# Optimization experiments

Measured on AMD Instinct MI355X. Metric: run time of the kernel, lower is better.

The kernel has to match this reference:

```python
import jax, jax.numpy as jnp
import numpy as np

B, DIM, L, H, W = 4, 128, 256, 8, 8
N = L * H * W
D_INNER, D_STATE, D_CONV, DT_RANK = 128, 8, 4, 8


def _ln(x, w, b, eps=1e-5):
    m = x.mean(-1, keepdims=True)
    v = ((x - m) ** 2).mean(-1, keepdims=True)
    return (x - m) * jax.lax.rsqrt(v + eps) * w + b


def _mamba_fusion(x, z_in, p, i):
    # x, z_in: (B, N, DIM). x drives the SSM; z_in provides the cross-modal gate.
    u = x @ p['Wx'][i]                                    # (B, N, D_INNER)
    z = z_in @ p['Wz'][i]                                 # (B, N, D_INNER)
    # causal depthwise conv1d along tokens, kernel D_CONV (torch pad=k-1 then truncate)
    up = jnp.pad(u, ((0, 0), (D_CONV - 1, 0), (0, 0)))
    w = p['conv_w'][i]                                    # (D_INNER, D_CONV)
    uc = sum(up[:, k:k + u.shape[1], :] * w[:, k] for k in range(D_CONV)) + p['conv_b'][i]
    uc = jax.nn.silu(uc)
    x_dbl = uc @ p['Wxproj'][i]                           # (B, N, DT_RANK + 2*D_STATE)
    dt_r, Bm, Cm = jnp.split(x_dbl, [DT_RANK, DT_RANK + D_STATE], axis=-1)
    dt = jax.nn.softplus(dt_r @ p['Wdt'][i] + p['bdt'][i])  # (B, N, D_INNER)
    A = -jnp.exp(p['A_log'][i])                           # (D_INNER, D_STATE)
    dA = jnp.exp(dt[..., None] * A)                       # (B, N, D_INNER, D_STATE)
    dBu = dt[..., None] * Bm[:, :, None, :] * uc[..., None]

    def step(h, inp):
        dA_t, dBu_t, C_t = inp
        h = dA_t * h + dBu_t                              # (B, D_INNER, D_STATE)
        return h, jnp.einsum('bds,bs->bd', h, C_t)

    h0 = jnp.zeros((u.shape[0], D_INNER, D_STATE), u.dtype)
    _, ys = jax.lax.scan(step, h0, (dA.swapaxes(0, 1), dBu.swapaxes(0, 1), Cm.swapaxes(0, 1)))
    y = ys.swapaxes(0, 1) + p['Dp'][i] * uc
    y = y * jax.nn.silu(z)
    return y @ p['Wout_m'][i] + p['bout_m'][i]


def _cross_block(in0, in1, p, i):
    skip = in0
    a = _ln(in0, p['ln0_w'][i], p['ln0_b'][i])
    b = _ln(in1, p['ln1_w'][i], p['ln1_b'][i])
    return skip + _mamba_fusion(a, b, p, i)


def setup_inputs() -> dict:
    key = jax.random.key(0)
    ks = jax.random.split(key, 16)
    s_in = 1.0 / np.sqrt(DIM)
    s_di = 1.0 / np.sqrt(D_INNER)
    inp = {
        'front': jax.random.normal(ks[0], (B, DIM, L, H, W), jnp.float32),
        'back': jax.random.normal(ks[1], (B, DIM, L, H, W), jnp.float32),
        'ln0_w': jnp.ones((2, DIM), jnp.float32),
        'ln0_b': jnp.zeros((2, DIM), jnp.float32),
        'ln1_w': jnp.ones((2, DIM), jnp.float32),
        'ln1_b': jnp.zeros((2, DIM), jnp.float32),
        'Wx': jax.random.normal(ks[2], (2, DIM, D_INNER), jnp.float32) * s_in,
        'Wz': jax.random.normal(ks[3], (2, DIM, D_INNER), jnp.float32) * s_in,
        'conv_w': jax.random.normal(ks[4], (2, D_INNER, D_CONV), jnp.float32) * 0.5,
        'conv_b': jnp.zeros((2, D_INNER), jnp.float32),
        'Wxproj': jax.random.normal(ks[5], (2, D_INNER, DT_RANK + 2 * D_STATE), jnp.float32) * s_di,
        'Wdt': jax.random.normal(ks[6], (2, DT_RANK, D_INNER), jnp.float32) * (1.0 / np.sqrt(DT_RANK)),
        'bdt': jnp.full((2, D_INNER), -4.6, jnp.float32),  # softplus^-1(~0.01)
        'A_log': jnp.broadcast_to(jnp.log(jnp.arange(1, D_STATE + 1, dtype=jnp.float32)), (2, D_INNER, D_STATE)).copy(),
        'Dp': jnp.ones((2, D_INNER), jnp.float32),
        'Wout_m': jax.random.normal(ks[7], (2, D_INNER, DIM), jnp.float32) * s_di,
        'bout_m': jnp.zeros((2, DIM), jnp.float32),
        'Wout': jax.random.normal(ks[8], (DIM, DIM), jnp.float32) * s_in,
        'bout': jnp.zeros((DIM,), jnp.float32),
    }
    return inp


def reference(front, back, ln0_w, ln0_b, ln1_w, ln1_b, Wx, Wz, conv_w, conv_b,
              Wxproj, Wdt, bdt, A_log, Dp, Wout_m, bout_m, Wout, bout):
    p = dict(ln0_w=ln0_w, ln0_b=ln0_b, ln1_w=ln1_w, ln1_b=ln1_b, Wx=Wx, Wz=Wz,
             conv_w=conv_w, conv_b=conv_b, Wxproj=Wxproj, Wdt=Wdt, bdt=bdt,
             A_log=A_log, Dp=Dp, Wout_m=Wout_m, bout_m=bout_m)
    ff = front.reshape(B, DIM, N).swapaxes(1, 2)          # (B, N, DIM)
    bf = back.reshape(B, DIM, N).swapaxes(1, 2)
    f_fus = _cross_block(ff, bf, p, 0)
    b_fus = _cross_block(bf, ff, p, 1)
    fusion = ((f_fus + b_fus) * 0.5) @ Wout + bout
    return fusion.swapaxes(1, 2).reshape(B, DIM, L, H, W)
```

## Files before the change

kernel.cpp:

```cpp
#include <hip/hip_runtime.h>

#define DEV static __device__ __forceinline__

typedef short s16x8 __attribute__((ext_vector_type(8)));
typedef float f32x4 __attribute__((ext_vector_type(4)));
typedef unsigned short u16;

DEV float b2f(u16 u){ return __uint_as_float(((unsigned int)u) << 16); }
DEV u16 f2b(float f){
  unsigned int x = __float_as_uint(f);
  x += 0x7fffu + ((x >> 16) & 1u);
  return (u16)(x >> 16);
}
DEV float silu_f(float x){ return x * __builtin_amdgcn_rcpf(1.f + __expf(-x)); }
DEV float softplus_f(float x){ return (x > 15.f) ? x : __logf(1.f + __expf(x)); }
DEV bool detf32(const void* lnw){ return *(const unsigned int*)lnw == 0x3F800000u; }
DEV float ldin(const void* p, long long i, bool f){
  return f ? ((const float*)p)[i] : b2f(((const u16*)p)[i]);
}

static constexpr int BATCH = 4;
static constexpr int NSEQ  = 16384;
static constexpr int RTOT  = BATCH * NSEQ;
static constexpr int GCH   = 256;
static constexpr int DIRSZ = BATCH*GCH*128*8;

__global__ __launch_bounds__(256) void k_setup(
                        const void* ln0w, const void* ln0b, const void* ln1w, const void* ln1b,
                        const void* Wx, const void* Wz, const void* Wxp, const void* Wdt,
                        const void* bdt, const void* Alog, const void* convw, const void* convb,
                        const void* Dpr, const void* Woutm, const void* boutm,
                        const void* Wout, const void* bout,
                        u16* Wuz, u16* WdtBC, u16* Wcat, u16* WoutT,
                        float* buz, float* bdtf, float* bcat, float* boutf,
                        float* Aexp, float* convwF, float* convbF, float* DpF)
{
  bool f = detf32(ln0w);
  int tid = blockIdx.x * 256 + threadIdx.x;
  int gs  = gridDim.x * 256;
  for (int idx = tid; idx < 2*256*128; idx += gs){
    int d = idx >> 15; int n = (idx >> 7) & 255; int k = idx & 127;
    float wv;
    if (n < 128) wv = ldin(ln0w, d*128+k, f) * ldin(Wx, (long long)(d*128+k)*128 + n, f);
    else         wv = ldin(ln1w, (1-d)*128+k, f) * ldin(Wz, (long long)((1-d)*128+k)*128 + (n-128), f);
    Wuz[idx] = f2b(wv);
  }
  for (int idx = tid; idx < 2*256; idx += gs){
    int d = idx >> 8; int n = idx & 255;
    float s = 0.f;
    if (n < 128){
      for (int k = 0; k < 128; ++k)
        s += ldin(ln0b, d*128+k, f) * ldin(Wx, (long long)(d*128+k)*128 + n, f);
    } else {
      for (int k = 0; k < 128; ++k)
        s += ldin(ln1b, (1-d)*128+k, f) * ldin(Wz, (long long)((1-d)*128+k)*128 + (n-128), f);
    }
    buz[idx] = s;
  }
  for (int idx = tid; idx < 2*128; idx += gs)
    bdtf[idx] = ldin(bdt, idx, f);
  for (int idx = tid; idx < 2*144*128; idx += gs){
    int i = idx / (144*128); int rem = idx % (144*128); int n = rem >> 7; int k = rem & 127;
    if (n < 128){
      float s = 0.f;
      for (int j = 0; j < 8; ++j)
        s += ldin(Wxp, (long long)(i*128+k)*24 + j, f) * ldin(Wdt, (long long)(i*8+j)*128 + n, f);
      WdtBC[idx] = f2b(s);
    } else {
      WdtBC[idx] = f2b(ldin(Wxp, (long long)(i*128+k)*24 + (n - 120), f));
    }
  }
  for (int idx = tid; idx < 128*256; idx += gs){
    int n = idx >> 8; int k = idx & 255;
    Wcat[idx] = f2b(ldin(Woutm, (long long)k*128 + n, f));
  }
  for (int idx = tid; idx < 128*128; idx += gs){
    int n = idx >> 7, k = idx & 127;
    WoutT[idx] = f2b(ldin(Wout, (long long)k*128 + n, f));
  }
  for (int idx = tid; idx < 128; idx += gs){
    bcat[idx]  = ldin(boutm, idx, f) + ldin(boutm, 128 + idx, f);
    boutf[idx] = ldin(bout, idx, f);
  }
  for (int idx = tid; idx < 2*128*8; idx += gs)
    Aexp[idx] = -expf(ldin(Alog, idx, f));
  for (int idx = tid; idx < 2*128*4; idx += gs)
    convwF[idx] = ldin(convw, idx, f);
  for (int idx = tid; idx < 2*128; idx += gs){
    convbF[idx] = ldin(convb, idx, f);
    DpF[idx]   = ldin(Dpr, idx, f);
  }
}

__global__ __launch_bounds__(256) void k_ln(const void* front, const void* back, const void* ln0w,
                                            u16* xf, u16* xb, u16* sfbh)
{
  bool fF = detf32(ln0w);
  __shared__ u16 Af[64][130];
  __shared__ u16 Ab[64][130];
  __shared__ float Mf[64], Rf[64], Mb[64], Rb[64];
  int tid = threadIdx.x;
  long long r0 = (long long)blockIdx.x * 64;
  int b  = (int)(r0 >> 14);
  int n0 = (int)(r0 & 16383);
  if (fF){
    const float* fp = (const float*)front;
    const float* bp = (const float*)back;
    for (int it = 0; it < 8; ++it){
      int d = it*16 + (tid >> 4);
      int t = (tid & 15) * 4;
      long long gi = ((long long)(b*128 + d))*NSEQ + n0 + t;
      float4 vf = *(const float4*)&fp[gi];
      float4 vb = *(const float4*)&bp[gi];
      Af[t+0][d] = f2b(vf.x); Af[t+1][d] = f2b(vf.y);
      Af[t+2][d] = f2b(vf.z); Af[t+3][d] = f2b(vf.w);
      Ab[t+0][d] = f2b(vb.x); Ab[t+1][d] = f2b(vb.y);
      Ab[t+2][d] = f2b(vb.z); Ab[t+3][d] = f2b(vb.w);
    }
  } else {
    const u16* fp = (const u16*)front;
    const u16* bp = (const u16*)back;
    for (int it = 0; it < 4; ++it){
      int d = it*32 + (tid >> 3);
      int t = (tid & 7) * 8;
      long long gi = ((long long)(b*128 + d))*NSEQ + n0 + t;
      uint4 vf = *(const uint4*)&fp[gi];
      uint4 vb = *(const uint4*)&bp[gi];
      Af[t+0][d] = (u16)vf.x; Af[t+1][d] = (u16)(vf.x>>16);
      Af[t+2][d] = (u16)vf.y; Af[t+3][d] = (u16)(vf.y>>16);
      Af[t+4][d] = (u16)vf.z; Af[t+5][d] = (u16)(vf.z>>16);
      Af[t+6][d] = (u16)vf.w; Af[t+7][d] = (u16)(vf.w>>16);
      Ab[t+0][d] = (u16)vb.x; Ab[t+1][d] = (u16)(vb.x>>16);
      Ab[t+2][d] = (u16)vb.y; Ab[t+3][d] = (u16)(vb.y>>16);
      Ab[t+4][d] = (u16)vb.z; Ab[t+5][d] = (u16)(vb.z>>16);
      Ab[t+6][d] = (u16)vb.w; Ab[t+7][d] = (u16)(vb.w>>16);
    }
  }
  __syncthreads();
  {
    int t = tid >> 2, sub = tid & 3;
    float s = 0.f, ss = 0.f, s2 = 0.f, ss2 = 0.f;
    for (int k = 0; k < 32; ++k){
      float v = b2f(Af[t][sub*32 + k]); s  += v; ss  += v*v;
      float w = b2f(Ab[t][sub*32 + k]); s2 += w; ss2 += w*w;
    }
    for (int m = 1; m < 4; m <<= 1){
      s  += __shfl_xor(s,  m, 64); ss  += __shfl_xor(ss,  m, 64);
      s2 += __shfl_xor(s2, m, 64); ss2 += __shfl_xor(ss2, m, 64);
    }
    if (sub == 0){
      float mf = s  * (1.f/128.f); float vf = ss  * (1.f/128.f) - mf*mf;
      Mf[t] = mf; Rf[t] = rsqrtf(vf + 1e-5f);
      float mb = s2 * (1.f/128.f); float vb = ss2 * (1.f/128.f) - mb*mb;
      Mb[t] = mb; Rb[t] = rsqrtf(vb + 1e-5f);
    }
  }
  __syncthreads();
  for (int it = 0; it < 8; ++it){
    int t = it*8 + (tid >> 5);
    int c = (tid & 31) * 4;
    float mf = Mf[t], rf = Rf[t], mb = Mb[t], rb = Rb[t];
    float f0 = b2f(Af[t][c+0]), f1 = b2f(Af[t][c+1]), f2 = b2f(Af[t][c+2]), f3 = b2f(Af[t][c+3]);
    float g0 = b2f(Ab[t][c+0]), g1 = b2f(Ab[t][c+1]), g2 = b2f(Ab[t][c+2]), g3 = b2f(Ab[t][c+3]);
    ushort4 xo, zo, so;
    xo.x = f2b((f0-mf)*rf); xo.y = f2b((f1-mf)*rf); xo.z = f2b((f2-mf)*rf); xo.w = f2b((f3-mf)*rf);
    zo.x = f2b((g0-mb)*rb); zo.y = f2b((g1-mb)*rb); zo.z = f2b((g2-mb)*rb); zo.w = f2b((g3-mb)*rb);
    so.x = f2b(f0+g0); so.y = f2b(f1+g1); so.z = f2b(f2+g2); so.w = f2b(f3+g3);
    long long o = (r0 + t)*128 + c;
    *(ushort4*)&xf[o] = xo;
    *(ushort4*)&xb[o] = zo;
    *(ushort4*)&sfbh[o] = so;
  }
}

__global__ __launch_bounds__(256) void k_guz(const u16* __restrict__ xf,
                                             const u16* __restrict__ xb,
                                             const u16* __restrict__ Wuz,
                                             const float* __restrict__ buz,
                                             u16* __restrict__ u0, u16* __restrict__ u1,
                                             u16* __restrict__ z0, u16* __restrict__ z1)
{
  int dir = blockIdx.y;
  const u16* A = dir ? xb : xf;
  const u16* Wt = Wuz + dir*256*128;
  const float* bias = buz + dir*256;
  u16* outU = dir ? u1 : u0;
  u16* outZ = dir ? z0 : z1;
  __shared__ u16 Wl[256][72];
  __shared__ u16 Al[64][72];
  int tid = threadIdx.x;
  long long r0 = (long long)blockIdx.x * 64;
  int w = tid >> 6, lane = tid & 63;
  int q = lane >> 4, m = lane & 15;
  f32x4 acc[16];
  #pragma unroll
  for (int ct = 0; ct < 16; ++ct) acc[ct] = (f32x4){0.f,0.f,0.f,0.f};
  for (int kp = 0; kp < 2; ++kp){
    if (kp) __syncthreads();
    for (int ci = tid; ci < 256*8; ci += 256){
      int n = ci >> 3, c8 = ci & 7;
      *(uint4*)&Wl[n][c8*8] = *(const uint4*)&Wt[n*128 + kp*64 + c8*8];
    }
    for (int ci = tid; ci < 64*8; ci += 256){
      int rl = ci >> 3, c8 = ci & 7;
      *(uint4*)&Al[rl][c8*8] = *(const uint4*)&A[(r0 + rl)*128 + kp*64 + c8*8];
    }
    __syncthreads();
    #pragma unroll
    for (int kt = 0; kt < 2; ++kt){
      s16x8 af = *(const s16x8*)&Al[w*16 + m][kt*32 + q*8];
      #pragma unroll
      for (int ct = 0; ct < 16; ++ct){
        s16x8 bf = *(const s16x8*)&Wl[ct*16 + m][kt*32 + q*8];
        acc[ct] = __builtin_amdgcn_mfma_f32_16x16x32_bf16(af, bf, acc[ct], 0, 0, 0);
      }
    }
  }
  #pragma unroll
  for (int ct = 0; ct < 16; ++ct){
    int col = ct*16 + m;
    #pragma unroll
    for (int i = 0; i < 4; ++i){
      long long r = r0 + w*16 + q*4 + i;
      float v = acc[ct][i] + bias[col];
      if (col < 128) outU[r*128 + col] = f2b(v);
      else           outZ[r*128 + (col - 128)] = f2b(silu_f(v));
    }
  }
}

__global__ __launch_bounds__(256) void k_cps(const u16* __restrict__ u0p,
                                             const u16* __restrict__ u1p,
                                             const float* __restrict__ convwF,
                                             const float* __restrict__ convbF,
                                             const u16* __restrict__ WdtBC,
                                             const float* __restrict__ bdtf,
                                             const float* __restrict__ Aexp,
                                             u16* __restrict__ uc0p, u16* __restrict__ uc1p,
                                             u16* __restrict__ yg,
                                             float* __restrict__ BCg,
                                             float* __restrict__ P, float* __restrict__ Q)
{
  __shared__ u16 Al[64][136];
  __shared__ u16 Wl[144][136];
  __shared__ float BCl[64][16];
  int dir = blockIdx.y;
  const u16* u = dir ? u1p : u0p;
  u16* ucb = dir ? uc1p : uc0p;
  const u16* Wt = WdtBC + dir*18432;
  const float* bias = bdtf + dir*128;
  u16* dtb = yg + dir*128;
  float* BC = BCg + (long long)dir*RTOT*16;
  int tid = threadIdx.x;
  long long r0 = (long long)blockIdx.x * 64;
  int b  = (int)(r0 >> 14);
  int n0 = (int)(r0 & 16383);
  for (int ci = tid; ci < 144*16; ci += 256){
    int n = ci >> 4, c8 = ci & 15;
    *(uint4*)&Wl[n][c8*8] = *(const uint4*)&Wt[n*128 + c8*8];
  }
  {
    int c = tid & 127, h = tid >> 7;
    const float* wp = &convwF[(dir*128 + c)*4];
    float w0 = wp[0], w1 = wp[1], w2 = wp[2], w3 = wp[3];
    float cb = convbF[dir*128 + c];
    int t0 = h*32;
    const u16* up = u + (long long)b*NSEQ*128 + c;
    int nbase = n0 + t0;
    float win0 = (nbase-3 >= 0) ? b2f(up[(long long)(nbase-3)*128]) : 0.f;
    float win1 = (nbase-2 >= 0) ? b2f(up[(long long)(nbase-2)*128]) : 0.f;
    float win2 = (nbase-1 >= 0) ? b2f(up[(long long)(nbase-1)*128]) : 0.f;
    #pragma unroll
    for (int t = 0; t < 32; ++t){
      float cur = b2f(up[(long long)(nbase + t)*128]);
      float a = win0*w0 + win1*w1 + win2*w2 + cur*w3 + cb;
      u16 s = f2b(silu_f(a));
      Al[t0 + t][c] = s;
      ucb[(r0 + t0 + t)*128 + c] = s;
      win0 = win1; win1 = win2; win2 = cur;
    }
  }
  __syncthreads();
  int w = tid >> 6, lane = tid & 63;
  int q = lane >> 4, m = lane & 15;
  f32x4 acc[9];
  #pragma unroll
  for (int ct = 0; ct < 9; ++ct) acc[ct] = (f32x4){0.f,0.f,0.f,0.f};
  #pragma unroll
  for (int kt = 0; kt < 4; ++kt){
    s16x8 af = *(const s16x8*)&Al[w*16 + m][kt*32 + q*8];
    #pragma unroll
    for (int ct = 0; ct < 9; ++ct){
      s16x8 bf = *(const s16x8*)&Wl[ct*16 + m][kt*32 + q*8];
      acc[ct] = __builtin_amdgcn_mfma_f32_16x16x32_bf16(af, bf, acc[ct], 0, 0, 0);
    }
  }
  __syncthreads();
  u16* Dl = (u16*)&Wl[0][0];
  #pragma unroll
  for (int ct = 0; ct < 9; ++ct){
    int col = ct*16 + m;
    #pragma unroll
    for (int i = 0; i < 4; ++i){
      int rl = w*16 + q*4 + i;
      long long r = r0 + rl;
      float v = acc[ct][i];
      if (col < 128){
        u16 dv = f2b(softplus_f(v + bias[col]));
        dtb[r*256 + col] = dv;
        Dl[rl*136 + col] = dv;
      } else {
        BC[r*16 + (col - 128)] = v;
        BCl[rl][col - 128] = v;
      }
    }
  }
  __syncthreads();
  {
    int c = tid & 127, sh = tid >> 7;
    int g = (int)(r0 & 16383) >> 6;
    float Ac[4], Pr[4], H[4];
    #pragma unroll
    for (int j = 0; j < 4; ++j){
      Ac[j] = Aexp[(dir*128 + c)*8 + sh*4 + j];
      Pr[j] = 1.f; H[j] = 0.f;
    }
    for (int t = 0; t < 64; ++t){
      float d  = b2f(Dl[t*136 + c]);
      float uu = b2f(Al[t][c]);
      float du = d * uu;
      #pragma unroll
      for (int j = 0; j < 4; ++j){
        float dA = __expf(d * Ac[j]);
        H[j]  = dA*H[j] + du*BCl[t][sh*4 + j];
        Pr[j] *= dA;
      }
    }
    long long o = (long long)dir*DIRSZ + (((long long)b*GCH + g)*128 + c)*8 + sh*4;
    *(float4*)&P[o] = make_float4(Pr[0],Pr[1],Pr[2],Pr[3]);
    *(float4*)&Q[o] = make_float4(H[0],H[1],H[2],H[3]);
  }
}

__global__ __launch_bounds__(64) void k_scan2(const float* __restrict__ P,
                                              const float* __restrict__ Q,
                                              float* __restrict__ hinit)
{
  int idx = blockIdx.x*64 + threadIdx.x;
  int dir = idx >> 12;
  int rem = idx & 4095;
  int b  = rem >> 10;
  int cs = rem & 1023;
  long long base = (long long)dir*DIRSZ + (long long)b*GCH*1024 + cs;
  float h = 0.f;
  for (int g = 0; g < GCH; g += 8){
    long long o = base + (long long)g*1024;
    float p[8], qv[8];
    #pragma unroll
    for (int j = 0; j < 8; ++j){ p[j] = P[o + j*1024]; qv[j] = Q[o + j*1024]; }
    #pragma unroll
    for (int j = 0; j < 8; ++j){
      hinit[o + j*1024] = h;
      h = p[j]*h + qv[j];
    }
  }
}

__global__ __launch_bounds__(256) void k_scan3(const u16* __restrict__ uc0p,
                                               const u16* __restrict__ uc1p,
                                               const float* __restrict__ BCg,
                                               const float* __restrict__ hinit,
                                               const u16* __restrict__ z0p,
                                               const u16* __restrict__ z1p,
                                               const float* __restrict__ DpF,
                                               const float* __restrict__ Aexp,
                                               u16* yg)
{
  __shared__ float Bl[128][8];
  __shared__ float Cl[128][8];
  int dir = blockIdx.y;
  const u16* uc = dir ? uc1p : uc0p;
  const u16* zs = dir ? z1p : z0p;
  const float* BC = BCg + (long long)dir*RTOT*16;
  int tid = threadIdx.x;
  int gp = blockIdx.x & 127;
  int b  = blockIdx.x >> 7;
  long long tokbase = (long long)b*NSEQ + gp*128;
  for (int idx = tid; idx < 128*8; idx += 256){
    int row = idx >> 3, s = idx & 7;
    Bl[row][s] = BC[(tokbase + row)*16 + s];
    Cl[row][s] = BC[(tokbase + row)*16 + 8 + s];
  }
  __syncthreads();
  int c = tid & 127;
  int gh = tid >> 7;
  int g = gp*2 + gh;
  int doff = dir*128;
  float Ac[8], H[8];
  long long ho = (long long)dir*DIRSZ + (((long long)b*GCH + g)*128 + c)*8;
  float4 h0 = *(const float4*)&hinit[ho];
  float4 h1 = *(const float4*)&hinit[ho + 4];
  H[0]=h0.x; H[1]=h0.y; H[2]=h0.z; H[3]=h0.w;
  H[4]=h1.x; H[5]=h1.y; H[6]=h1.z; H[7]=h1.w;
  #pragma unroll
  for (int s = 0; s < 8; ++s) Ac[s] = Aexp[(dir*128 + c)*8 + s];
  float dpc = DpF[dir*128 + c];
  long long rbase = (long long)b*NSEQ + g*64;
  for (int t = 0; t < 64; ++t){
    long long r = rbase + t;
    float d  = b2f(yg[r*256 + doff + c]);
    float uu = b2f(uc[r*128 + c]);
    float du = d * uu;
    int rowl = gh*64 + t;
    float y = 0.f;
    #pragma unroll
    for (int s = 0; s < 8; ++s){
      float dA = __expf(d * Ac[s]);
      H[s] = dA*H[s] + du*Bl[rowl][s];
      y += H[s]*Cl[rowl][s];
    }
    float zv = b2f(zs[r*128 + c]);
    yg[r*256 + doff + c] = f2b((y + dpc*uu) * zv);
  }
}

__global__ __launch_bounds__(256) void k_tail(const u16* __restrict__ yg,
                                              const u16* __restrict__ Wcat,
                                              const float* __restrict__ bcat,
                                              const u16* __restrict__ sfbh,
                                              const u16* __restrict__ WoutT,
                                              const float* __restrict__ boutf,
                                              void* outp, const void* dflag)
{
  __shared__ u16 Wl[128][136];
  __shared__ u16 Al[64][136];
  __shared__ u16 Sl[64][136];
  int tid = threadIdx.x;
  long long r0 = (long long)blockIdx.x * 64;
  int w = tid >> 6, lane = tid & 63;
  int q = lane >> 4, m = lane & 15;
  f32x4 acc[8];
  #pragma unroll
  for (int ct = 0; ct < 8; ++ct) acc[ct] = (f32x4){0.f,0.f,0.f,0.f};
  for (int kp = 0; kp < 2; ++kp){
    if (kp) __syncthreads();
    for (int ci = tid; ci < 128*16; ci += 256){
      int n = ci >> 4, c8 = ci & 15;
      *(uint4*)&Wl[n][c8*8] = *(const uint4*)&Wcat[n*256 + kp*128 + c8*8];
    }
    for (int ci = tid; ci < 64*16; ci += 256){
      int rl = ci >> 4, c8 = ci & 15;
      *(uint4*)&Al[rl][c8*8] = *(const uint4*)&yg[(r0 + rl)*256 + kp*128 + c8*8];
    }
    __syncthreads();
    #pragma unroll
    for (int kt = 0; kt < 4; ++kt){
      s16x8 af = *(const s16x8*)&Al[w*16 + m][kt*32 + q*8];
      #pragma unroll
      for (int ct = 0; ct < 8; ++ct){
        s16x8 bf = *(const s16x8*)&Wl[ct*16 + m][kt*32 + q*8];
        acc[ct] = __builtin_amdgcn_mfma_f32_16x16x32_bf16(af, bf, acc[ct], 0, 0, 0);
      }
    }
  }
  #pragma unroll
  for (int ct = 0; ct < 8; ++ct){
    int col = ct*16 + m;
    #pragma unroll
    for (int i = 0; i < 4; ++i){
      int rl = w*16 + q*4 + i;
      long long r = r0 + rl;
      Sl[rl][col] = f2b(acc[ct][i] + bcat[col] + b2f(sfbh[r*128 + col]));
    }
  }
  __syncthreads();
  for (int ci = tid; ci < 128*16; ci += 256){
    int n = ci >> 4, c8 = ci & 15;
    *(uint4*)&Wl[n][c8*8] = *(const uint4*)&WoutT[n*128 + c8*8];
  }
  __syncthreads();
  f32x4 acc2[8];
  #pragma unroll
  for (int ct = 0; ct < 8; ++ct) acc2[ct] = (f32x4){0.f,0.f,0.f,0.f};
  #pragma unroll
  for (int kt = 0; kt < 4; ++kt){
    s16x8 af = *(const s16x8*)&Sl[w*16 + m][kt*32 + q*8];
    #pragma unroll
    for (int ct = 0; ct < 8; ++ct){
      s16x8 bf = *(const s16x8*)&Wl[ct*16 + m][kt*32 + q*8];
      acc2[ct] = __builtin_amdgcn_mfma_f32_16x16x32_bf16(af, bf, acc2[ct], 0, 0, 0);
    }
  }
  u16* Tl = &Al[0][0];
  #pragma unroll
  for (int ct = 0; ct < 8; ++ct){
    int col = ct*16 + m;
    #pragma unroll
    for (int i = 0; i < 4; ++i){
      int rl = w*16 + q*4 + i;
      Tl[col*68 + rl] = f2b(0.5f*acc2[ct][i] + boutf[col]);
    }
  }
  __syncthreads();
  long long b = r0 >> 14; long long tok0 = r0 & 16383;
  bool fo = detf32(dflag);
  if (fo){
    float* of = (float*)outp;
    for (int idx = tid; idx < 128*16; idx += 256){
      int n = idx >> 4; int t0 = (idx & 15)*4;
      float4 v;
      v.x = b2f(Tl[n*68 + t0+0]); v.y = b2f(Tl[n*68 + t0+1]);
      v.z = b2f(Tl[n*68 + t0+2]); v.w = b2f(Tl[n*68 + t0+3]);
      *(float4*)&of[(((long long)(b*128 + n)) << 14) + tok0 + t0] = v;
    }
  } else {
    u16* ob = (u16*)outp;
    for (int idx = tid; idx < 128*16; idx += 256){
      int n = idx >> 4; int t0 = (idx & 15)*4;
      ushort4 v;
      v.x = Tl[n*68 + t0+0]; v.y = Tl[n*68 + t0+1];
      v.z = Tl[n*68 + t0+2]; v.w = Tl[n*68 + t0+3];
      *(ushort4*)&ob[(((long long)(b*128 + n)) << 14) + tok0 + t0] = v;
    }
  }
}

extern "C" void kernel_launch(void* const* d_in, const int* in_sizes, int n_in,
                              void* d_out, int out_size, void* d_ws, size_t ws_size,
                              hipStream_t stream)
{
  (void)in_sizes; (void)n_in; (void)out_size; (void)ws_size;
  const void* front = d_in[0];
  const void* back  = d_in[1];
  const void* ln0w  = d_in[2];
  const void* ln0b  = d_in[3];
  const void* ln1w  = d_in[4];
  const void* ln1b  = d_in[5];
  const void* Wx    = d_in[6];
  const void* Wz    = d_in[7];
  const void* convw = d_in[8];
  const void* convb = d_in[9];
  const void* Wxp   = d_in[10];
  const void* Wdt   = d_in[11];
  const void* bdt   = d_in[12];
  const void* Alog  = d_in[13];
  const void* Dpr   = d_in[14];
  const void* Woutm = d_in[15];
  const void* boutm = d_in[16];
  const void* Wout  = d_in[17];
  const void* bout  = d_in[18];

  char* p = (char*)d_ws;
  auto alloc = [&](size_t bytes) -> void* {
    void* q = (void*)p; p += (bytes + 255) & ~(size_t)255; return q;
  };
  u16*   xf    = (u16*)  alloc((size_t)RTOT*128*2);
  u16*   xb    = (u16*)  alloc((size_t)RTOT*128*2);
  u16*   sfbh  = (u16*)  alloc((size_t)RTOT*128*2);
  u16*   u0    = (u16*)  alloc((size_t)RTOT*128*2);
  u16*   u1    = (u16*)  alloc((size_t)RTOT*128*2);
  u16*   z0    = (u16*)  alloc((size_t)RTOT*128*2);
  u16*   z1    = (u16*)  alloc((size_t)RTOT*128*2);
  float* BC    = (float*)alloc((size_t)2*RTOT*16*4);
  float* Pb    = (float*)alloc((size_t)2*DIRSZ*4);
  float* Qb    = (float*)alloc((size_t)2*DIRSZ*4);
  float* hin   = (float*)alloc((size_t)2*DIRSZ*4);
  u16*   yg    = (u16*)  alloc((size_t)RTOT*256*2);
  u16*   Wuz   = (u16*)  alloc(2*256*128*2);
  u16*   WdtBC = (u16*)  alloc(2*144*128*2);
  u16*   Wcat  = (u16*)  alloc(128*256*2);
  u16*   WoutT = (u16*)  alloc(128*128*2);
  float* buz   = (float*)alloc(2*256*4);
  float* bdtf  = (float*)alloc(2*128*4);
  float* bcat  = (float*)alloc(128*4);
  float* boutf = (float*)alloc(128*4);
  float* Aexp  = (float*)alloc(2*128*8*4);
  float* convwF= (float*)alloc(2*128*4*4);
  float* convbF= (float*)alloc(2*128*4);
  float* DpF   = (float*)alloc(2*128*4);

  k_setup<<<128,256,0,stream>>>(ln0w,ln0b,ln1w,ln1b,Wx,Wz,Wxp,Wdt,bdt,Alog,convw,convb,Dpr,
                                Woutm,boutm,Wout,bout,
                                Wuz,WdtBC,Wcat,WoutT,buz,bdtf,bcat,boutf,Aexp,
                                convwF,convbF,DpF);
  k_ln<<<RTOT/64,256,0,stream>>>(front,back,ln0w,xf,xb,sfbh);

  dim3 g2(RTOT/64, 2);
  k_guz<<<g2,256,0,stream>>>(xf, xb, Wuz, buz, u0, u1, z0, z1);
  k_cps<<<g2,256,0,stream>>>(u0, u1, convwF, convbF, WdtBC, bdtf, Aexp,
                             xf, xb, yg, BC, Pb, Qb);
  k_scan2<<<128,64,0,stream>>>(Pb, Qb, hin);
  dim3 g3(BATCH*GCH/2, 2);
  k_scan3<<<g3,256,0,stream>>>(xf, xb, BC, hin, z0, z1, DpF, Aexp, yg);
  k_tail<<<RTOT/64,256,0,stream>>>(yg, Wcat, bcat, sfbh, WoutT, boutf, d_out, ln0w);
}
```

Before: 347.5 us.

## Widen chunk-scan parallelism, use exp2 with prescaled A, transpose LDS tiles

k_cps now runs 512 threads per block. It splits the conv across four 16-token segments and the MFMA columns across two warp groups. The chunk-local scan uses a swizzled transposed LDS layout and two states per thread, and computes the decay product as exp2(A*sum(dt)) instead of a running product. k_scan3 launches one block per 64-token chunk with two lanes per channel, each holding four states, and combines them with a shuffle. A is premultiplied by log2(e) so exp2 replaces exp. The intent is to raise occupancy and parallelism in the scan stages, at the cost of more blocks, shuffles and LDS aliasing complexity.

```diff
diff --git a/kernel.cpp b/kernel.cpp
--- a/kernel.cpp
+++ b/kernel.cpp
@@ -23,7 +23,7 @@
 static constexpr int NSEQ  = 16384;
 static constexpr int RTOT  = BATCH * NSEQ;
 static constexpr int GCH   = 256;
-static constexpr int DIRSZ = BATCH*GCH*128*8;
+static constexpr long long DIRSZ = (long long)BATCH*GCH*128*8;
 
 __global__ __launch_bounds__(256) void k_setup(
                         const void* ln0w, const void* ln0b, const void* ln1w, const void* ln1b,
@@ -33,7 +33,7 @@
                         const void* Wout, const void* bout,
                         u16* Wuz, u16* WdtBC, u16* Wcat, u16* WoutT,
                         float* buz, float* bdtf, float* bcat, float* boutf,
-                        float* Aexp, float* convwF, float* convbF, float* DpF)
+                        float* Aexp2, float* convwF, float* convbF, float* DpF)
 {
   bool f = detf32(ln0w);
   int tid = blockIdx.x * 256 + threadIdx.x;
@@ -83,7 +83,7 @@
     boutf[idx] = ldin(bout, idx, f);
   }
   for (int idx = tid; idx < 2*128*8; idx += gs)
-    Aexp[idx] = -expf(ldin(Alog, idx, f));
+    Aexp2[idx] = -expf(ldin(Alog, idx, f)) * 1.44269504f;
   for (int idx = tid; idx < 2*128*4; idx += gs)
     convwF[idx] = ldin(convw, idx, f);
   for (int idx = tid; idx < 2*128; idx += gs){
@@ -229,13 +229,26 @@
   }
 }
 
-__global__ __launch_bounds__(256) void k_cps(const u16* __restrict__ u0p,
+DEV uint4 pack8(const u16* v){
+  uint4 r;
+  r.x = (unsigned)v[0] | ((unsigned)v[1]<<16);
+  r.y = (unsigned)v[2] | ((unsigned)v[3]<<16);
+  r.z = (unsigned)v[4] | ((unsigned)v[5]<<16);
+  r.w = (unsigned)v[6] | ((unsigned)v[7]<<16);
+  return r;
+}
+DEV void unpack8(uint4 v, u16* o){
+  o[0]=(u16)v.x; o[1]=(u16)(v.x>>16); o[2]=(u16)v.y; o[3]=(u16)(v.y>>16);
+  o[4]=(u16)v.z; o[5]=(u16)(v.z>>16); o[6]=(u16)v.w; o[7]=(u16)(v.w>>16);
+}
+
+__global__ __launch_bounds__(512) void k_cps(const u16* __restrict__ u0p,
                                              const u16* __restrict__ u1p,
                                              const float* __restrict__ convwF,
                                              const float* __restrict__ convbF,
                                              const u16* __restrict__ WdtBC,
                                              const float* __restrict__ bdtf,
-                                             const float* __restrict__ Aexp,
+                                             const float* __restrict__ Aexp2,
                                              u16* __restrict__ uc0p, u16* __restrict__ uc1p,
                                              u16* __restrict__ yg,
                                              float* __restrict__ BCg,
@@ -243,7 +256,9 @@
 {
   __shared__ u16 Al[64][136];
   __shared__ u16 Wl[144][136];
-  __shared__ float BCl[64][16];
+  __shared__ uint4 UcT4[128*8];
+  float* BCs = (float*)&Al[0][0];
+  uint4* DlT4 = (uint4*)&Wl[0][0];
   int dir = blockIdx.y;
   const u16* u = dir ? u1p : u0p;
   u16* ucb = dir ? uc1p : uc0p;
@@ -255,7 +270,7 @@
   long long r0 = (long long)blockIdx.x * 64;
   int b  = (int)(r0 >> 14);
   int n0 = (int)(r0 & 16383);
-  for (int ci = tid; ci < 144*16; ci += 256){
+  for (int ci = tid; ci < 144*16; ci += 512){
     int n = ci >> 4, c8 = ci & 15;
     *(uint4*)&Wl[n][c8*8] = *(const uint4*)&Wt[n*128 + c8*8];
   }
@@ -264,81 +279,110 @@
     const float* wp = &convwF[(dir*128 + c)*4];
     float w0 = wp[0], w1 = wp[1], w2 = wp[2], w3 = wp[3];
     float cb = convbF[dir*128 + c];
-    int t0 = h*32;
+    int t0 = h*16;
     const u16* up = u + (long long)b*NSEQ*128 + c;
     int nbase = n0 + t0;
     float win0 = (nbase-3 >= 0) ? b2f(up[(long long)(nbase-3)*128]) : 0.f;
     float win1 = (nbase-2 >= 0) ? b2f(up[(long long)(nbase-2)*128]) : 0.f;
     float win2 = (nbase-1 >= 0) ? b2f(up[(long long)(nbase-1)*128]) : 0.f;
-    #pragma unroll
-    for (int t = 0; t < 32; ++t){
+    u16 tmp[16];
+    #pragma unroll
+    for (int t = 0; t < 16; ++t){
       float cur = b2f(up[(long long)(nbase + t)*128]);
       float a = win0*w0 + win1*w1 + win2*w2 + cur*w3 + cb;
       u16 s = f2b(silu_f(a));
+      tmp[t] = s;
       Al[t0 + t][c] = s;
       ucb[(r0 + t0 + t)*128 + c] = s;
       win0 = win1; win1 = win2; win2 = cur;
     }
+    UcT4[c*8 + ((h*2+0) ^ (c&7))] = pack8(tmp);
+    UcT4[c*8 + ((h*2+1) ^ (c&7))] = pack8(tmp+8);
   }
   __syncthreads();
   int w = tid >> 6, lane = tid & 63;
   int q = lane >> 4, m = lane & 15;
-  f32x4 acc[9];
-  #pragma unroll
-  for (int ct = 0; ct < 9; ++ct) acc[ct] = (f32x4){0.f,0.f,0.f,0.f};
+  int rt = w & 3;
+  int cg = w >> 2;
+  int ct0 = cg ? 5 : 0;
+  int nct = cg ? 4 : 5;
+  f32x4 acc[5];
+  #pragma unroll
+  for (int j = 0; j < 5; ++j) acc[j] = (f32x4){0.f,0.f,0.f,0.f};
   #pragma unroll
   for (int kt = 0; kt < 4; ++kt){
-    s16x8 af = *(const s16x8*)&Al[w*16 + m][kt*32 + q*8];
-    #pragma unroll
-    for (int ct = 0; ct < 9; ++ct){
-      s16x8 bf = *(const s16x8*)&Wl[ct*16 + m][kt*32 + q*8];
-      acc[ct] = __builtin_amdgcn_mfma_f32_16x16x32_bf16(af, bf, acc[ct], 0, 0, 0);
-    }
-  }
-  __syncthreads();
-  u16* Dl = (u16*)&Wl[0][0];
-  #pragma unroll
-  for (int ct = 0; ct < 9; ++ct){
-    int col = ct*16 + m;
-    #pragma unroll
-    for (int i = 0; i < 4; ++i){
-      int rl = w*16 + q*4 + i;
-      long long r = r0 + rl;
-      float v = acc[ct][i];
-      if (col < 128){
-        u16 dv = f2b(softplus_f(v + bias[col]));
-        dtb[r*256 + col] = dv;
-        Dl[rl*136 + col] = dv;
-      } else {
-        BC[r*16 + (col - 128)] = v;
-        BCl[rl][col - 128] = v;
+    s16x8 af = *(const s16x8*)&Al[rt*16 + m][kt*32 + q*8];
+    #pragma unroll
+    for (int j = 0; j < 5; ++j){
+      if (j < nct){
+        s16x8 bf = *(const s16x8*)&Wl[(ct0+j)*16 + m][kt*32 + q*8];
+        acc[j] = __builtin_amdgcn_mfma_f32_16x16x32_bf16(af, bf, acc[j], 0, 0, 0);
       }
     }
   }
   __syncthreads();
+  int rl0 = rt*16 + q*4;
+  #pragma unroll
+  for (int j = 0; j < 5; ++j){
+    if (j >= nct) continue;
+    int col = (ct0+j)*16 + m;
+    if (col < 128){
+      ushort4 dv;
+      u16 dd[4];
+      #pragma unroll
+      for (int i = 0; i < 4; ++i){
+        u16 v = f2b(softplus_f(acc[j][i] + bias[col]));
+        dd[i] = v;
+        dtb[(r0 + rl0 + i)*256 + col] = v;
+      }
+      dv.x=dd[0]; dv.y=dd[1]; dv.z=dd[2]; dv.w=dd[3];
+      u16* d16 = (u16*)DlT4;
+      *(ushort4*)&d16[((col*8 + ((rl0>>3) ^ (col&7)))<<3) + (rl0&7)] = dv;
+    } else {
+      int s = col - 128;
+      #pragma unroll
+      for (int i = 0; i < 4; ++i)
+        BC[(r0 + rl0 + i)*16 + s] = acc[j][i];
+      float4 bv; bv.x=acc[j][0]; bv.y=acc[j][1]; bv.z=acc[j][2]; bv.w=acc[j][3];
+      *(float4*)&BCs[s*68 + rl0] = bv;
+    }
+  }
+  __syncthreads();
   {
-    int c = tid & 127, sh = tid >> 7;
+    int c = tid & 127, sq = tid >> 7;
+    int s0 = sq*2;
+    float Ac0 = Aexp2[(dir*128 + c)*8 + s0];
+    float Ac1 = Aexp2[(dir*128 + c)*8 + s0 + 1];
+    float H0 = 0.f, H1 = 0.f, sd = 0.f;
+    #pragma unroll
+    for (int g8 = 0; g8 < 8; ++g8){
+      int gi = c*8 + (g8 ^ (c&7));
+      u16 uu8[8], dd8[8];
+      unpack8(UcT4[gi], uu8);
+      unpack8(DlT4[gi], dd8);
+      float4 b0a = *(const float4*)&BCs[s0*68 + g8*8];
+      float4 b0b = *(const float4*)&BCs[s0*68 + g8*8 + 4];
+      float4 b1a = *(const float4*)&BCs[(s0+1)*68 + g8*8];
+      float4 b1b = *(const float4*)&BCs[(s0+1)*68 + g8*8 + 4];
+      const float* p0 = &b0a.x;
+      const float* p1 = &b1a.x;
+      #pragma unroll
+      for (int jj = 0; jj < 8; ++jj){
+        float d  = b2f(dd8[jj]);
+        float du = d * b2f(uu8[jj]);
+        sd += d;
+        float B0 = (jj < 4) ? p0[jj] : (&b0b.x)[jj-4];
+        float B1 = (jj < 4) ? p1[jj] : (&b1b.x)[jj-4];
+        H0 = __builtin_exp2f(d*Ac0)*H0 + du*B0;
+        H1 = __builtin_exp2f(d*Ac1)*H1 + du*B1;
+      }
+    }
     int g = (int)(r0 & 16383) >> 6;
-    float Ac[4], Pr[4], H[4];
-    #pragma unroll
-    for (int j = 0; j < 4; ++j){
-      Ac[j] = Aexp[(dir*128 + c)*8 + sh*4 + j];
-      Pr[j] = 1.f; H[j] = 0.f;
-    }
-    for (int t = 0; t < 64; ++t){
-      float d  = b2f(Dl[t*136 + c]);
-      float uu = b2f(Al[t][c]);
-      float du = d * uu;
-      #pragma unroll
-      for (int j = 0; j < 4; ++j){
-        float dA = __expf(d * Ac[j]);
-        H[j]  = dA*H[j] + du*BCl[t][sh*4 + j];
-        Pr[j] *= dA;
-      }
-    }
-    long long o = (long long)dir*DIRSZ + (((long long)b*GCH + g)*128 + c)*8 + sh*4;
-    *(float4*)&P[o] = make_float4(Pr[0],Pr[1],Pr[2],Pr[3]);
-    *(float4*)&Q[o] = make_float4(H[0],H[1],H[2],H[3]);
+    long long o = (long long)dir*DIRSZ + (((long long)b*GCH + g)*128 + c)*8 + s0;
+    P[o]   = __builtin_exp2f(Ac0*sd);
+    P[o+1] = __builtin_exp2f(Ac1*sd);
+    Q[o]   = H0;
+    Q[o+1] = H1;
   }
 }
 
@@ -373,54 +417,56 @@
                                                const u16* __restrict__ z0p,
                                                const u16* __restrict__ z1p,
                                                const float* __restrict__ DpF,
-                                               const float* __restrict__ Aexp,
+                                               const float* __restrict__ Aexp2,
                                                u16* yg)
 {
-  __shared__ float Bl[128][8];
-  __shared__ float Cl[128][8];
+  __shared__ float Bl[64][8];
+  __shared__ float Cl[64][8];
   int dir = blockIdx.y;
   const u16* uc = dir ? uc1p : uc0p;
   const u16* zs = dir ? z1p : z0p;
   const float* BC = BCg + (long long)dir*RTOT*16;
   int tid = threadIdx.x;
-  int gp = blockIdx.x & 127;
-  int b  = blockIdx.x >> 7;
-  long long tokbase = (long long)b*NSEQ + gp*128;
-  for (int idx = tid; idx < 128*8; idx += 256){
+  int b = blockIdx.x >> 8;
+  int g = blockIdx.x & 255;
+  long long rbase = (long long)b*NSEQ + g*64;
+  for (int idx = tid; idx < 64*8; idx += 256){
     int row = idx >> 3, s = idx & 7;
-    Bl[row][s] = BC[(tokbase + row)*16 + s];
-    Cl[row][s] = BC[(tokbase + row)*16 + 8 + s];
-  }
-  __syncthreads();
-  int c = tid & 127;
-  int gh = tid >> 7;
-  int g = gp*2 + gh;
+    Bl[row][s] = BC[(rbase + row)*16 + s];
+    Cl[row][s] = BC[(rbase + row)*16 + 8 + s];
+  }
+  __syncthreads();
+  int wv = tid >> 6, l = tid & 63;
+  int c = wv*32 + (l >> 1);
+  int sh = l & 1;
   int doff = dir*128;
-  float Ac[8], H[8];
-  long long ho = (long long)dir*DIRSZ + (((long long)b*GCH + g)*128 + c)*8;
-  float4 h0 = *(const float4*)&hinit[ho];
-  float4 h1 = *(const float4*)&hinit[ho + 4];
-  H[0]=h0.x; H[1]=h0.y; H[2]=h0.z; H[3]=h0.w;
-  H[4]=h1.x; H[5]=h1.y; H[6]=h1.z; H[7]=h1.w;
-  #pragma unroll
-  for (int s = 0; s < 8; ++s) Ac[s] = Aexp[(dir*128 + c)*8 + s];
+  float Ac[4], H[4];
+  #pragma unroll
+  for (int j = 0; j < 4; ++j) Ac[j] = Aexp2[(dir*128 + c)*8 + sh*4 + j];
+  long long ho = (long long)dir*DIRSZ + (((long long)b*GCH + g)*128 + c)*8 + sh*4;
+  float4 h4 = *(const float4*)&hinit[ho];
+  H[0]=h4.x; H[1]=h4.y; H[2]=h4.z; H[3]=h4.w;
   float dpc = DpF[dir*128 + c];
-  long long rbase = (long long)b*NSEQ + g*64;
   for (int t = 0; t < 64; ++t){
     long long r = rbase + t;
     float d  = b2f(yg[r*256 + doff + c]);
     float uu = b2f(uc[r*128 + c]);
     float du = d * uu;
-    int rowl = gh*64 + t;
-    float y = 0.f;
-    #pragma unroll
-    for (int s = 0; s < 8; ++s){
-      float dA = __expf(d * Ac[s]);
-      H[s] = dA*H[s] + du*Bl[rowl][s];
-      y += H[s]*Cl[rowl][s];
-    }
-    float zv = b2f(zs[r*128 + c]);
-    yg[r*256 + doff + c] = f2b((y + dpc*uu) * zv);
+    float4 bt = *(const float4*)&Bl[t][sh*4];
+    float4 ct = *(const float4*)&Cl[t][sh*4];
+    float y;
+    {
+      float e0 = __builtin_exp2f(d*Ac[0]); H[0] = e0*H[0] + du*bt.x;
+      float e1 = __builtin_exp2f(d*Ac[1]); H[1] = e1*H[1] + du*bt.y;
+      float e2 = __builtin_exp2f(d*Ac[2]); H[2] = e2*H[2] + du*bt.z;
+      float e3 = __builtin_exp2f(d*Ac[3]); H[3] = e3*H[3] + du*bt.w;
+      y = H[0]*ct.x + H[1]*ct.y + H[2]*ct.z + H[3]*ct.w;
+    }
+    y += __shfl_xor(y, 1, 64);
+    if (sh == 0){
+      float zv = b2f(zs[r*128 + c]);
+      yg[r*256 + doff + c] = f2b((y + dpc*uu) * zv);
+    }
   }
 }
 
@@ -574,23 +620,23 @@
   float* bdtf  = (float*)alloc(2*128*4);
   float* bcat  = (float*)alloc(128*4);
   float* boutf = (float*)alloc(128*4);
-  float* Aexp  = (float*)alloc(2*128*8*4);
+  float* Aexp2 = (float*)alloc(2*128*8*4);
   float* convwF= (float*)alloc(2*128*4*4);
   float* convbF= (float*)alloc(2*128*4);
   float* DpF   = (float*)alloc(2*128*4);
 
   k_setup<<<128,256,0,stream>>>(ln0w,ln0b,ln1w,ln1b,Wx,Wz,Wxp,Wdt,bdt,Alog,convw,convb,Dpr,
                                 Woutm,boutm,Wout,bout,
-                                Wuz,WdtBC,Wcat,WoutT,buz,bdtf,bcat,boutf,Aexp,
+                                Wuz,WdtBC,Wcat,WoutT,buz,bdtf,bcat,boutf,Aexp2,
                                 convwF,convbF,DpF);
   k_ln<<<RTOT/64,256,0,stream>>>(front,back,ln0w,xf,xb,sfbh);
 
   dim3 g2(RTOT/64, 2);
   k_guz<<<g2,256,0,stream>>>(xf, xb, Wuz, buz, u0, u1, z0, z1);
-  k_cps<<<g2,256,0,stream>>>(u0, u1, convwF, convbF, WdtBC, bdtf, Aexp,
+  k_cps<<<g2,512,0,stream>>>(u0, u1, convwF, convbF, WdtBC, bdtf, Aexp2,
                              xf, xb, yg, BC, Pb, Qb);
   k_scan2<<<128,64,0,stream>>>(Pb, Qb, hin);
-  dim3 g3(BATCH*GCH/2, 2);
-  k_scan3<<<g3,256,0,stream>>>(xf, xb, BC, hin, z0, z1, DpF, Aexp, yg);
+  dim3 g3(BATCH*GCH, 2);
+  k_scan3<<<g3,256,0,stream>>>(xf, xb, BC, hin, z0, z1, DpF, Aexp2, yg);
   k_tail<<<RTOT/64,256,0,stream>>>(yg, Wcat, bcat, sfbh, WoutT, boutf, d_out, ln0w);
 }
```

New measurement: 371.5 us. +6.9%, slower.
